# Kernel optimization log

Measured on AMD Instinct MI355X. Metric: run time of the kernel, lower is better.

The kernel has to match this reference:

```python
import jax, jax.numpy as jnp
import numpy as np
from jax import lax

B, S, H = 2, 2048, 768
FF = 1536
E = 8
TOP_K = 2


def setup_inputs() -> dict:
    key = jax.random.key(0)
    k1, k2, k3, k4 = jax.random.split(key, 4)
    hidden_states = jax.random.normal(k1, (B, S, H), dtype=jnp.float32)
    # torch init: weight.normal_() for experts; nn.Linear default init for gate (approx normal here is fine for a numerics baseline)
    gate_w = jax.random.normal(k2, (E, H), dtype=jnp.float32) * 0.02
    w_fc = jax.random.normal(k3, (E, FF, H), dtype=jnp.float32) * 0.02
    w_proj = jax.random.normal(k4, (E, H, FF), dtype=jnp.float32) * 0.02
    return {"hidden_states": hidden_states, "gate_w": gate_w, "w_fc": w_fc, "w_proj": w_proj}


def reference(hidden_states, gate_w, w_fc, w_proj):
    b, s, h = hidden_states.shape
    x = hidden_states.reshape(-1, h)                      # [T, H]
    # --- top-k gating (logits in float32, as in the torch code) ---
    logits = (x @ gate_w.T).astype(jnp.float32)           # [T, E]
    top_logits, top_idx = lax.top_k(logits, TOP_K)        # [T, K]
    gates = jax.nn.softmax(top_logits, axis=1).astype(x.dtype)  # [T, K]
    # combined per-token/per-expert gate: g[t,e] = sum_k gates[t,k]*[idx[t,k]==e]
    onehot = jax.nn.one_hot(top_idx, E, dtype=x.dtype)    # [T, K, E]
    g = jnp.einsum('tk,tke->te', gates, onehot)           # [T, E]
    # --- experts: gather + per-expert GEMM + gated scatter-add combine ---
    # Equivalent math: tokens with zero gate for expert e contribute nothing,
    # so compute each expert on all tokens and weight by g[:, e].
    out = jnp.zeros_like(x)
    for e in range(E):  # fixed small loop over experts (structurally distinct weights)
        hmid = jax.nn.gelu(x @ w_fc[e].T, approximate=False)   # [T, FF] (torch gelu = erf form)
        out = out + g[:, e:e + 1] * (hmid @ w_proj[e].T)       # [T, H]
    out = out.reshape(b, s, h)
    return out, logits
```

## Files before the change

### kernel.cpp

```cpp
#include <hip/hip_runtime.h>
#include <hip/hip_bf16.h>
#include <math.h>
#include <stdint.h>

#define TOKENS 4096
#define HDIM   768
#define FFDIM  1536
#define NEXP   8

typedef __attribute__((ext_vector_type(8))) short bf16x8;
typedef __attribute__((ext_vector_type(4))) float f32x4;

__device__ __forceinline__ unsigned short f2bf(float f) {
    union { float f; uint32_t u; } c; c.f = f;
    uint32_t u = c.u;
    uint32_t r = (u + 0x7FFFu + ((u >> 16) & 1u)) >> 16;
    return (unsigned short)r;
}

__device__ __forceinline__ void gload_lds16(const void* g, void* l) {
    __builtin_amdgcn_global_load_lds(
        (const __attribute__((address_space(1))) void*)g,
        (__attribute__((address_space(3))) void*)l, 16, 0, 0);
}

__global__ void zero_init(float* __restrict__ outp, int n) {
    int i = blockIdx.x * blockDim.x + threadIdx.x;
    int stride = gridDim.x * blockDim.x;
    for (int j = i; j < n; j += stride) outp[j] = 0.f;
}

__global__ void cast_bf16(const float* __restrict__ src,
                          unsigned short* __restrict__ dst, int n4) {
    int stride = gridDim.x * blockDim.x;
    for (int i = blockIdx.x * blockDim.x + threadIdx.x; i < n4; i += stride) {
        float4 v = ((const float4*)src)[i];
        ushort4 o;
        o.x = f2bf(v.x); o.y = f2bf(v.y); o.z = f2bf(v.z); o.w = f2bf(v.w);
        ((ushort4*)dst)[i] = o;
    }
}

__global__ __launch_bounds__(256) void gating(
    const float* __restrict__ x, const float* __restrict__ gw,
    float* __restrict__ logits,
    int* __restrict__ tok_e, float* __restrict__ tok_g,
    unsigned short* __restrict__ x_bf)
{
    int t = blockIdx.x * 4 + (threadIdx.x >> 6);
    int lane = threadIdx.x & 63;
    const float4* xt = (const float4*)(x + (size_t)t * HDIM);
    const float4* gw4 = (const float4*)gw;
    ushort4* xbt = (ushort4*)(x_bf + (size_t)t * HDIM);
    float acc[NEXP];
#pragma unroll
    for (int e = 0; e < NEXP; e++) acc[e] = 0.f;
#pragma unroll
    for (int it = 0; it < 3; it++) {
        int i = lane + it * 64;
        float4 xv = xt[i];
        ushort4 o;
        o.x = f2bf(xv.x); o.y = f2bf(xv.y); o.z = f2bf(xv.z); o.w = f2bf(xv.w);
        xbt[i] = o;
#pragma unroll
        for (int e = 0; e < NEXP; e++) {
            float4 wv = gw4[e * 192 + i];
            acc[e] += xv.x * wv.x + xv.y * wv.y + xv.z * wv.z + xv.w * wv.w;
        }
    }
#pragma unroll
    for (int e = 0; e < NEXP; e++) {
#pragma unroll
        for (int off = 32; off > 0; off >>= 1)
            acc[e] += __shfl_xor(acc[e], off);
    }
    if (lane == 0) {
        float4 l0 = make_float4(acc[0], acc[1], acc[2], acc[3]);
        float4 l1 = make_float4(acc[4], acc[5], acc[6], acc[7]);
        float4* lp = (float4*)(logits + (size_t)t * NEXP);
        lp[0] = l0; lp[1] = l1;
        int i0 = 0; float v0 = acc[0];
#pragma unroll
        for (int e = 1; e < NEXP; e++) if (acc[e] > v0) { v0 = acc[e]; i0 = e; }
        int i1 = -1; float v1 = -3.4e38f;
#pragma unroll
        for (int e = 0; e < NEXP; e++) if (e != i0 && acc[e] > v1) { v1 = acc[e]; i1 = e; }
        float g0 = 1.f / (1.f + expf(v1 - v0));
        tok_e[t * 2] = i0; tok_e[t * 2 + 1] = i1;
        tok_g[t * 2] = g0; tok_g[t * 2 + 1] = 1.f - g0;
    }
}

__global__ __launch_bounds__(1024) void build_lists(
    const int* __restrict__ tok_e, const float* __restrict__ tok_g,
    int* __restrict__ counts, int* __restrict__ bases,
    int* __restrict__ entries, float* __restrict__ gates)
{
    __shared__ unsigned long long slo[1024], shi[1024];
    int tid = threadIdx.x;
    int eL[8]; float gL[8];
    int4 ea = ((const int4*)tok_e)[tid * 2];
    int4 eb = ((const int4*)tok_e)[tid * 2 + 1];
    float4 ga = ((const float4*)tok_g)[tid * 2];
    float4 gb = ((const float4*)tok_g)[tid * 2 + 1];
    eL[0] = ea.x; eL[1] = ea.y; eL[2] = ea.z; eL[3] = ea.w;
    eL[4] = eb.x; eL[5] = eb.y; eL[6] = eb.z; eL[7] = eb.w;
    gL[0] = ga.x; gL[1] = ga.y; gL[2] = ga.z; gL[3] = ga.w;
    gL[4] = gb.x; gL[5] = gb.y; gL[6] = gb.z; gL[7] = gb.w;

    unsigned long long clo = 0, chi = 0;
#pragma unroll
    for (int j = 0; j < 8; j++) {
        int e = eL[j];
        unsigned long long one = 1ull << ((e & 3) * 16);
        if (e < 4) clo += one; else chi += one;
    }
    slo[tid] = clo; shi[tid] = chi;
    __syncthreads();
    for (int s = 1; s < 1024; s <<= 1) {
        unsigned long long vlo = 0, vhi = 0;
        if (tid >= s) { vlo = slo[tid - s]; vhi = shi[tid - s]; }
        __syncthreads();
        slo[tid] += vlo; shi[tid] += vhi;
        __syncthreads();
    }
    unsigned long long rlo = slo[tid] - clo;
    unsigned long long rhi = shi[tid] - chi;
    if (tid == 0) {
        unsigned long long tlo = slo[1023], thi = shi[1023];
        int c[8];
#pragma unroll
        for (int e = 0; e < 4; e++) {
            c[e]     = (int)((tlo >> (e * 16)) & 0xFFFF);
            c[e + 4] = (int)((thi >> (e * 16)) & 0xFFFF);
        }
        int b = 0;
#pragma unroll
        for (int e = 0; e < NEXP; e++) { counts[e] = c[e]; bases[e] = b; b += c[e]; }
    }
#pragma unroll
    for (int j = 0; j < 8; j++) {
        int e = eL[j];
        int sh = (e & 3) * 16;
        unsigned long long one = 1ull << sh;
        int slot;
        if (e < 4) { slot = (int)((rlo >> sh) & 0xFFFF); rlo += one; }
        else       { slot = (int)((rhi >> sh) & 0xFFFF); rhi += one; }
        entries[e * TOKENS + slot] = tid * 8 + j;
        gates[e * TOKENS + slot]   = gL[j];
    }
}

template<int KD, int ND, bool IS_FC>
__global__ __launch_bounds__(256) void moe_gemm(
    const unsigned short* __restrict__ Asrc,
    const unsigned short* __restrict__ Bsrc,
    const int* __restrict__ counts,
    const int* __restrict__ bases,
    const int* __restrict__ entries,
    const float* __restrict__ gates,
    unsigned short* __restrict__ hmid,
    float* __restrict__ outp)
{
    int e = blockIdx.z;
    int n_e = counts[e];
    int rowTile = blockIdx.y;
    if (rowTile * 128 >= n_e) return;
    int ebase = bases[e];
    int n0 = blockIdx.x * 128;

    __shared__ __align__(16) unsigned short sA[128 * 32];
    __shared__ __align__(16) unsigned short sB[128 * 32];

    int tid = threadIdx.x;
    int w = tid >> 6;
    int l = tid & 63;
    const int* lst = entries + e * TOKENS;

    int r0 = w * 32 + (l >> 2);
    int r1 = r0 + 16;
    int p  = l & 3;
    int ss0 = p ^ ((r0 >> 1) & 3);
    int ss1 = p ^ ((r1 >> 1) & 3);

    int lr0 = rowTile * 128 + r0;
    int lr1 = rowTile * 128 + r1;
    int id0 = lr0 < n_e ? lr0 : n_e - 1;
    int id1 = lr1 < n_e ? lr1 : n_e - 1;
    size_t arow0, arow1;
    if (IS_FC) { arow0 = (size_t)(lst[id0] >> 1); arow1 = (size_t)(lst[id1] >> 1); }
    else       { arow0 = (size_t)(ebase + id0);   arow1 = (size_t)(ebase + id1);   }

    const unsigned short* Ag0 = Asrc + arow0 * KD + ss0 * 8;
    const unsigned short* Ag1 = Asrc + arow1 * KD + ss1 * 8;
    const unsigned short* Bg0 = Bsrc + ((size_t)e * ND + n0 + r0) * KD + ss0 * 8;
    const unsigned short* Bg1 = Bsrc + ((size_t)e * ND + n0 + r1) * KD + ss1 * 8;
    unsigned short* sA0 = sA + (2 * w)     * 512;
    unsigned short* sA1 = sA + (2 * w + 1) * 512;
    unsigned short* sB0 = sB + (2 * w)     * 512;
    unsigned short* sB1 = sB + (2 * w + 1) * 512;

    int lo = l & 15;
    int q  = l >> 4;
    int wr = w >> 1, wc = w & 1;
    int aOff[4], bOff[4];
#pragma unroll
    for (int i = 0; i < 4; i++) {
        int m = wr * 64 + i * 16 + lo;
        aOff[i] = m * 32 + (q ^ ((m >> 1) & 3)) * 8;
        int n = wc * 64 + i * 16 + lo;
        bOff[i] = n * 32 + (q ^ ((n >> 1) & 3)) * 8;
    }

    f32x4 acc[4][4];
#pragma unroll
    for (int i = 0; i < 4; i++)
#pragma unroll
        for (int j = 0; j < 4; j++) acc[i][j] = (f32x4){0.f, 0.f, 0.f, 0.f};

    for (int k0 = 0; k0 < KD; k0 += 32) {
        gload_lds16(Ag0 + k0, sA0);
        gload_lds16(Ag1 + k0, sA1);
        gload_lds16(Bg0 + k0, sB0);
        gload_lds16(Bg1 + k0, sB1);
        __syncthreads();
        bf16x8 a[4], b[4];
#pragma unroll
        for (int i = 0; i < 4; i++) a[i] = *(const bf16x8*)(sA + aOff[i]);
#pragma unroll
        for (int j = 0; j < 4; j++) b[j] = *(const bf16x8*)(sB + bOff[j]);
#pragma unroll
        for (int i = 0; i < 4; i++)
#pragma unroll
            for (int j = 0; j < 4; j++)
                acc[i][j] = __builtin_amdgcn_mfma_f32_16x16x32_bf16(a[i], b[j], acc[i][j], 0, 0, 0);
        __syncthreads();
    }

#pragma unroll
    for (int i = 0; i < 4; i++) {
        int rowB = rowTile * 128 + wr * 64 + i * 16 + q * 4;
#pragma unroll
        for (int rr = 0; rr < 4; rr++) {
            int orow = rowB + rr;
            if (orow < n_e) {
                if (IS_FC) {
                    size_t hrow = (size_t)(ebase + orow);
#pragma unroll
                    for (int j = 0; j < 4; j++) {
                        float v = acc[i][j][rr];
                        v = 0.5f * v * (1.f + erff(v * 0.70710678118654752f));
                        hmid[hrow * ND + n0 + wc * 64 + j * 16 + lo] = f2bf(v);
                    }
                } else {
                    int token = lst[orow] >> 1;
                    float g = gates[e * TOKENS + orow];
#pragma unroll
                    for (int j = 0; j < 4; j++) {
                        atomicAdd(&outp[(size_t)token * ND + n0 + wc * 64 + j * 16 + lo],
                                  acc[i][j][rr] * g);
                    }
                }
            }
        }
    }
}

extern "C" void kernel_launch(void* const* d_in, const int* in_sizes, int n_in,
                              void* d_out, int out_size, void* d_ws, size_t ws_size,
                              hipStream_t stream) {
    const float* x     = (const float*)d_in[0];
    const float* gw    = (const float*)d_in[1];
    const float* wfc   = (const float*)d_in[2];
    const float* wproj = (const float*)d_in[3];
    float* outp   = (float*)d_out;
    float* logits = outp + (size_t)TOKENS * HDIM;

    char* ws = (char*)d_ws;
    int*   counts  = (int*)ws;
    int*   bases   = (int*)(ws + 64);
    int*   entries = (int*)(ws + 256);
    float* gates   = (float*)(ws + 256 + NEXP * TOKENS * 4);
    size_t off = 256 + 2ull * NEXP * TOKENS * 4;
    int*   tok_e   = (int*)(ws + off);   off += (size_t)TOKENS * 2 * 4;
    float* tok_g   = (float*)(ws + off); off += (size_t)TOKENS * 2 * 4;
    unsigned short* x_bf   = (unsigned short*)(ws + off); off += (size_t)TOKENS * HDIM * 2;
    unsigned short* wfc_bf = (unsigned short*)(ws + off); off += (size_t)NEXP * FFDIM * HDIM * 2;
    unsigned short* wpj_bf = (unsigned short*)(ws + off); off += (size_t)NEXP * HDIM * FFDIM * 2;
    unsigned short* hmid   = (unsigned short*)(ws + off);

    zero_init<<<2048, 256, 0, stream>>>(outp, TOKENS * HDIM);
    cast_bf16<<<2048, 256, 0, stream>>>(wfc, wfc_bf, NEXP * FFDIM * HDIM / 4);
    cast_bf16<<<2048, 256, 0, stream>>>(wproj, wpj_bf, NEXP * HDIM * FFDIM / 4);
    gating<<<TOKENS / 4, 256, 0, stream>>>(x, gw, logits, tok_e, tok_g, x_bf);
    build_lists<<<1, 1024, 0, stream>>>(tok_e, tok_g, counts, bases, entries, gates);
    moe_gemm<HDIM, FFDIM, true ><<<dim3(FFDIM / 128, TOKENS / 128, NEXP), 256, 0, stream>>>(
        x_bf, wfc_bf, counts, bases, entries, gates, hmid, outp);
    moe_gemm<FFDIM, HDIM, false><<<dim3(HDIM / 128, TOKENS / 128, NEXP), 256, 0, stream>>>(
        hmid, wpj_bf, counts, bases, entries, gates, hmid, outp);
}
```

Baseline: 250.8 us.

## Compact MoE row tiles into a packed list, split-K the projection GEMM, fuse setup kernels

Builds a compact list of (expert, row-offset) tiles in build_lists so the GEMM grids launch only a bounded number of row tiles instead of a full tokens-by-experts grid of mostly-empty blocks. The projection GEMM is split along K into two halves, relying on the existing atomicAdd output to merge partials, which doubles the number of blocks for the small N dimension. Output zeroing moves into the gating kernel and the two weight casts merge into one launch, cutting kernel launches. The cost is doubled atomic traffic on the output and a hard cap of 72 tiles, which must cover the worst-case tile count.

```diff
diff --git a/kernel.cpp b/kernel.cpp
--- a/kernel.cpp
+++ b/kernel.cpp
@@ -7,6 +7,7 @@
 #define HDIM   768
 #define FFDIM  1536
 #define NEXP   8
+#define MAXRT  72
 
 typedef __attribute__((ext_vector_type(8))) short bf16x8;
 typedef __attribute__((ext_vector_type(4))) float f32x4;
@@ -24,20 +25,18 @@
         (__attribute__((address_space(3))) void*)l, 16, 0, 0);
 }
 
-__global__ void zero_init(float* __restrict__ outp, int n) {
-    int i = blockIdx.x * blockDim.x + threadIdx.x;
+__global__ void cast_bf16_2(const float* __restrict__ s1, unsigned short* __restrict__ d1,
+                            const float* __restrict__ s2, unsigned short* __restrict__ d2,
+                            int n4) {
     int stride = gridDim.x * blockDim.x;
-    for (int j = i; j < n; j += stride) outp[j] = 0.f;
-}
-
-__global__ void cast_bf16(const float* __restrict__ src,
-                          unsigned short* __restrict__ dst, int n4) {
-    int stride = gridDim.x * blockDim.x;
-    for (int i = blockIdx.x * blockDim.x + threadIdx.x; i < n4; i += stride) {
-        float4 v = ((const float4*)src)[i];
+    for (int i = blockIdx.x * blockDim.x + threadIdx.x; i < 2 * n4; i += stride) {
+        const float4* s = (i < n4) ? (const float4*)s1 : (const float4*)s2;
+        ushort4* d = (i < n4) ? (ushort4*)d1 : (ushort4*)d2;
+        int j = (i < n4) ? i : i - n4;
+        float4 v = s[j];
         ushort4 o;
         o.x = f2bf(v.x); o.y = f2bf(v.y); o.z = f2bf(v.z); o.w = f2bf(v.w);
-        ((ushort4*)dst)[i] = o;
+        d[j] = o;
     }
 }
 
@@ -45,8 +44,13 @@
     const float* __restrict__ x, const float* __restrict__ gw,
     float* __restrict__ logits,
     int* __restrict__ tok_e, float* __restrict__ tok_g,
-    unsigned short* __restrict__ x_bf)
+    unsigned short* __restrict__ x_bf, float* __restrict__ outp)
 {
+    float4 zz = make_float4(0.f, 0.f, 0.f, 0.f);
+#pragma unroll
+    for (int j = 0; j < 3; j++)
+        ((float4*)outp)[blockIdx.x * 768 + j * 256 + threadIdx.x] = zz;
+
     int t = blockIdx.x * 4 + (threadIdx.x >> 6);
     int lane = threadIdx.x & 63;
     const float4* xt = (const float4*)(x + (size_t)t * HDIM);
@@ -94,6 +98,7 @@
 __global__ __launch_bounds__(1024) void build_lists(
     const int* __restrict__ tok_e, const float* __restrict__ tok_g,
     int* __restrict__ counts, int* __restrict__ bases,
+    int* __restrict__ rtiles, int* __restrict__ nrt,
     int* __restrict__ entries, float* __restrict__ gates)
 {
     __shared__ unsigned long long slo[1024], shi[1024];
@@ -134,9 +139,13 @@
             c[e]     = (int)((tlo >> (e * 16)) & 0xFFFF);
             c[e + 4] = (int)((thi >> (e * 16)) & 0xFFFF);
         }
-        int b = 0;
-#pragma unroll
-        for (int e = 0; e < NEXP; e++) { counts[e] = c[e]; bases[e] = b; b += c[e]; }
+        int b = 0, nt = 0;
+#pragma unroll
+        for (int e = 0; e < NEXP; e++) {
+            counts[e] = c[e]; bases[e] = b; b += c[e];
+            for (int r = 0; r < c[e]; r += 128) rtiles[nt++] = (e << 16) | r;
+        }
+        nrt[0] = nt;
     }
 #pragma unroll
     for (int j = 0; j < 8; j++) {
@@ -151,21 +160,25 @@
     }
 }
 
-template<int KD, int ND, bool IS_FC>
+template<int KD, int ND, bool IS_FC, int KSPLIT>
 __global__ __launch_bounds__(256) void moe_gemm(
     const unsigned short* __restrict__ Asrc,
     const unsigned short* __restrict__ Bsrc,
     const int* __restrict__ counts,
     const int* __restrict__ bases,
+    const int* __restrict__ rtiles,
+    const int* __restrict__ nrt,
     const int* __restrict__ entries,
     const float* __restrict__ gates,
     unsigned short* __restrict__ hmid,
     float* __restrict__ outp)
 {
-    int e = blockIdx.z;
-    int n_e = counts[e];
-    int rowTile = blockIdx.y;
-    if (rowTile * 128 >= n_e) return;
+    int ti = blockIdx.y;
+    if (ti >= nrt[0]) return;
+    int pk   = rtiles[ti];
+    int e    = pk >> 16;
+    int row0 = pk & 0xFFFF;
+    int n_e  = counts[e];
     int ebase = bases[e];
     int n0 = blockIdx.x * 128;
 
@@ -183,8 +196,8 @@
     int ss0 = p ^ ((r0 >> 1) & 3);
     int ss1 = p ^ ((r1 >> 1) & 3);
 
-    int lr0 = rowTile * 128 + r0;
-    int lr1 = rowTile * 128 + r1;
+    int lr0 = row0 + r0;
+    int lr1 = row0 + r1;
     int id0 = lr0 < n_e ? lr0 : n_e - 1;
     int id1 = lr1 < n_e ? lr1 : n_e - 1;
     size_t arow0, arow1;
@@ -218,7 +231,9 @@
 #pragma unroll
         for (int j = 0; j < 4; j++) acc[i][j] = (f32x4){0.f, 0.f, 0.f, 0.f};
 
-    for (int k0 = 0; k0 < KD; k0 += 32) {
+    const int kBeg = (KD / KSPLIT) * blockIdx.z;
+    const int kEnd = kBeg + KD / KSPLIT;
+    for (int k0 = kBeg; k0 < kEnd; k0 += 32) {
         gload_lds16(Ag0 + k0, sA0);
         gload_lds16(Ag1 + k0, sA1);
         gload_lds16(Bg0 + k0, sB0);
@@ -239,7 +254,7 @@
 
 #pragma unroll
     for (int i = 0; i < 4; i++) {
-        int rowB = rowTile * 128 + wr * 64 + i * 16 + q * 4;
+        int rowB = row0 + wr * 64 + i * 16 + q * 4;
 #pragma unroll
         for (int rr = 0; rr < 4; rr++) {
             int orow = rowB + rr;
@@ -279,9 +294,11 @@
     char* ws = (char*)d_ws;
     int*   counts  = (int*)ws;
     int*   bases   = (int*)(ws + 64);
-    int*   entries = (int*)(ws + 256);
-    float* gates   = (float*)(ws + 256 + NEXP * TOKENS * 4);
-    size_t off = 256 + 2ull * NEXP * TOKENS * 4;
+    int*   nrt     = (int*)(ws + 128);
+    int*   rtiles  = (int*)(ws + 160);
+    int*   entries = (int*)(ws + 512);
+    float* gates   = (float*)(ws + 512 + NEXP * TOKENS * 4);
+    size_t off = 512 + 2ull * NEXP * TOKENS * 4;
     int*   tok_e   = (int*)(ws + off);   off += (size_t)TOKENS * 2 * 4;
     float* tok_g   = (float*)(ws + off); off += (size_t)TOKENS * 2 * 4;
     unsigned short* x_bf   = (unsigned short*)(ws + off); off += (size_t)TOKENS * HDIM * 2;
@@ -289,13 +306,13 @@
     unsigned short* wpj_bf = (unsigned short*)(ws + off); off += (size_t)NEXP * HDIM * FFDIM * 2;
     unsigned short* hmid   = (unsigned short*)(ws + off);
 
-    zero_init<<<2048, 256, 0, stream>>>(outp, TOKENS * HDIM);
-    cast_bf16<<<2048, 256, 0, stream>>>(wfc, wfc_bf, NEXP * FFDIM * HDIM / 4);
-    cast_bf16<<<2048, 256, 0, stream>>>(wproj, wpj_bf, NEXP * HDIM * FFDIM / 4);
-    gating<<<TOKENS / 4, 256, 0, stream>>>(x, gw, logits, tok_e, tok_g, x_bf);
-    build_lists<<<1, 1024, 0, stream>>>(tok_e, tok_g, counts, bases, entries, gates);
-    moe_gemm<HDIM, FFDIM, true ><<<dim3(FFDIM / 128, TOKENS / 128, NEXP), 256, 0, stream>>>(
-        x_bf, wfc_bf, counts, bases, entries, gates, hmid, outp);
-    moe_gemm<FFDIM, HDIM, false><<<dim3(HDIM / 128, TOKENS / 128, NEXP), 256, 0, stream>>>(
-        hmid, wpj_bf, counts, bases, entries, gates, hmid, outp);
-}
+    cast_bf16_2<<<2048, 256, 0, stream>>>(wfc, wfc_bf, wproj, wpj_bf,
+                                          NEXP * FFDIM * HDIM / 4);
+    gating<<<TOKENS / 4, 256, 0, stream>>>(x, gw, logits, tok_e, tok_g, x_bf, outp);
+    build_lists<<<1, 1024, 0, stream>>>(tok_e, tok_g, counts, bases, rtiles, nrt,
+                                        entries, gates);
+    moe_gemm<HDIM, FFDIM, true, 1><<<dim3(FFDIM / 128, MAXRT, 1), 256, 0, stream>>>(
+        x_bf, wfc_bf, counts, bases, rtiles, nrt, entries, gates, hmid, outp);
+    moe_gemm<FFDIM, HDIM, false, 2><<<dim3(HDIM / 128, MAXRT, 2), 256, 0, stream>>>(
+        hmid, wpj_bf, counts, bases, rtiles, nrt, entries, gates, hmid, outp);
+}
```

Measured after the change: 280.2 us. 11.7% more time.
